# Performance work log

Measured on AMD Instinct MI355X. Metric: run time of the kernel, lower is better.

Reference implementation:

```python
import jax, jax.numpy as jnp
import numpy as np

CODEBOOK_SIZE = 1024
EMBED_DIM = 256
LEVELS = 8
N_TOKENS = 65536


def setup_inputs() -> dict:
    key = jax.random.key(0)
    kx, kc = jax.random.split(key)
    x = jax.random.normal(kx, (N_TOKENS, EMBED_DIM), dtype=jnp.float32)
    # L codebooks, each [K, D], matching nn.Embedding default N(0,1) init
    codebooks = jax.random.normal(kc, (LEVELS, CODEBOOK_SIZE, EMBED_DIM), dtype=jnp.float32)
    return {"x": x, "codebooks": codebooks}


def reference(x, codebooks):
    # x: [N, D]; codebooks: [L, K, D]
    # Residual VQ: per level, nearest codebook entry via squared L2,
    # using the GEMM expansion ||r||^2 + ||c||^2 - 2 r.c (same argmin as
    # the naive broadcasted (r - c)^2 sum, without the [N, K, D] tensor).
    levels = codebooks.shape[0]
    residual = x
    quantized = jnp.zeros_like(x)
    codes = []
    for l in range(levels):
        cb = codebooks[l]                                  # [K, D]
        r_sq = jnp.sum(residual * residual, axis=1, keepdims=True)   # [N, 1]
        c_sq = jnp.sum(cb * cb, axis=1)[None, :]                      # [1, K]
        cross = jnp.einsum('nd,kd->nk', residual, cb)                 # [N, K]
        dists = r_sq + c_sq - 2.0 * cross                              # [N, K]
        idx = jnp.argmin(dists, axis=1)                                # [N]
        codes.append(idx)
        quant = cb[idx]                                                # [N, D]
        quantized = quantized + quant
        residual = residual - quant
    return quantized, jnp.stack(codes, axis=1)  # [N, D], [N, L]
```

## Files before the change

kernel.cpp:

```cpp
#include <hip/hip_runtime.h>

#define N_TOK 65536
#define DIM   256
#define KCB   1024
#define LVL   8
#define TPB   32
#define THREADS 1024
#define CAND_MAX 32
#define MARGIN_STAR 0.6f
#define MARGIN_F32  0.125f
#define RPAD  258

typedef __attribute__((ext_vector_type(8))) short bf16x8;
typedef __attribute__((ext_vector_type(4))) float f32x4;

static __device__ inline unsigned short f2bf(float f) {
    unsigned u = __float_as_uint(f);
    unsigned r = u + 0x7FFFu + ((u >> 16) & 1u);
    return (unsigned short)(r >> 16);
}

static __device__ inline unsigned fflip(float x) {
    unsigned u = __float_as_uint(x);
    return (u & 0x80000000u) ? ~u : (u | 0x80000000u);
}
static __device__ inline float funflip(unsigned u) {
    return __uint_as_float((u & 0x80000000u) ? (u & 0x7FFFFFFFu) : ~u);
}

__device__ __noinline__ double dist64(const double* r, const float* crow) {
    double s0 = 0.0, s1 = 0.0, s2 = 0.0, s3 = 0.0;
    #pragma unroll 8
    for (int d = 0; d < DIM; d += 4) {
        float4 c = *(const float4*)(crow + d);
        double a = r[d]     - (double)c.x;
        double b = r[d + 1] - (double)c.y;
        double e = r[d + 2] - (double)c.z;
        double f = r[d + 3] - (double)c.w;
        s0 += a * a; s1 += b * b; s2 += e * e; s3 += f * f;
    }
    return (s0 + s1) + (s2 + s3);
}

__global__ void pack_kernel(const float* __restrict__ cb, short* __restrict__ packed) {
    const int lane = threadIdx.x & 63;
    const int fid  = (blockIdx.x * blockDim.x + threadIdx.x) >> 6;
    const int l  = fid >> 9;
    const int n  = (fid >> 3) & 63;
    const int kk = fid & 7;
    const int col = n * 16 + (lane & 15);
    const int kb  = kk * 32 + (lane >> 4) * 8;
    const float* src = cb + ((long)(l * KCB + col)) * DIM + kb;
    float4 f0 = *(const float4*)src;
    float4 f1 = *(const float4*)(src + 4);
    float fv[8] = {f0.x, f0.y, f0.z, f0.w, f1.x, f1.y, f1.z, f1.w};
    union { unsigned short s[8]; int4 v; } H;
    #pragma unroll
    for (int j = 0; j < 8; j++) H.s[j] = f2bf(fv[j]);
    *(int4*)(packed + (long)fid * 512 + lane * 8) = H.v;
}

__global__ void bias_kernel(const float* __restrict__ cb, float* __restrict__ bias) {
    const int lane = threadIdx.x & 63;
    const int wid  = (blockIdx.x * blockDim.x + threadIdx.x) >> 6;
    const int nw   = (gridDim.x * blockDim.x) >> 6;
    for (int row = wid; row < LVL * KCB; row += nw) {
        float4 c = *(const float4*)(cb + (long)row * DIM + lane * 4);
        float s = c.x * c.x + c.y * c.y + c.z * c.z + c.w * c.w;
        for (int off = 32; off; off >>= 1) s += __shfl_xor(s, off);
        if (lane == 0) bias[row] = -0.5f * s;
    }
}

__global__ __launch_bounds__(THREADS, 4) void rvq_mfma(const float* __restrict__ x,
                                                       const float* __restrict__ cb,
                                                       const short* __restrict__ packed,
                                                       const float* __restrict__ bias,
                                                       float* __restrict__ out) {
    __shared__ short    abufH[2 * 8 * 64 * 8];
    __shared__ float    bias_s[KCB];
    __shared__ unsigned maxu[TPB];
    __shared__ int      ccnt[TPB];
    __shared__ int      clist[TPB][CAND_MAX];
    __shared__ int      codes_s[TPB][LVL];

    const int tid  = threadIdx.x;
    const int w    = tid >> 6;
    const int lane = tid & 63;
    const int tokq = tid >> 5;
    const int c32  = tid & 31;
    const long tok0 = (long)blockIdx.x * TPB;
    const float* xblk = x + tok0 * DIM;

    double res[8];
    #pragma unroll
    for (int p = 0; p < 4; p++) {
        float2 xv = *(const float2*)(xblk + tokq * DIM + 2 * c32 + 64 * p);
        res[2 * p]     = (double)xv.x;
        res[2 * p + 1] = (double)xv.y;
    }
    if (tid < TPB) { ccnt[tid] = 0; maxu[tid] = 0u; }
    bias_s[tid] = bias[tid];

    bf16x8 chA[4], chB[4];
    {
        const short* pack0 = packed + ((long)(w * 4) * 8) * 512 + lane * 8;
        #pragma unroll
        for (int n = 0; n < 4; n++) chA[n] = *(const bf16x8*)(pack0 + (long)(n * 8 + 0) * 512);
        #pragma unroll
        for (int n = 0; n < 4; n++) chB[n] = *(const bf16x8*)(pack0 + (long)(n * 8 + 1) * 512);
    }
    {
        const int m = tokq >> 4, tr = tokq & 15;
        #pragma unroll
        for (int p = 0; p < 4; p++) {
            int d = 2 * c32 + 64 * p;
            unsigned short hA = f2bf((float)res[2 * p]);
            unsigned short hB = f2bf((float)res[2 * p + 1]);
            int kk  = d >> 5;
            int ls  = tr + ((d >> 3) & 3) * 16;
            int idx = ((m * 8 + kk) * 64 + ls) * 8 + (d & 7);
            *(unsigned*)&abufH[idx] = (unsigned)hA | ((unsigned)hB << 16);
        }
    }
    __syncthreads();

    for (int l = 0; l < LVL; l++) {
        const float* cbl = cb + (long)l * KCB * DIM;

        const short* packW = packed + ((long)(l * 64 + w * 4) * 8) * 512 + lane * 8;
        f32x4 acc[2][4];
        #pragma unroll
        for (int n = 0; n < 4; n++) {
            float b = bias_s[w * 64 + n * 16 + (lane & 15)];
            acc[0][n] = (f32x4){b, b, b, b};
            acc[1][n] = (f32x4){b, b, b, b};
        }
        #pragma unroll
        for (int kk2 = 0; kk2 < 8; kk2 += 2) {
            {
                bf16x8 ah0 = *(const bf16x8*)(abufH + (kk2)     * 512 + lane * 8);
                bf16x8 ah1 = *(const bf16x8*)(abufH + (8 + kk2) * 512 + lane * 8);
                #pragma unroll
                for (int n = 0; n < 4; n++) {
                    acc[0][n] = __builtin_amdgcn_mfma_f32_16x16x32_bf16(ah0, chA[n], acc[0][n], 0, 0, 0);
                    acc[1][n] = __builtin_amdgcn_mfma_f32_16x16x32_bf16(ah1, chA[n], acc[1][n], 0, 0, 0);
                }
            }
            if (kk2 + 2 < 8) {
                #pragma unroll
                for (int n = 0; n < 4; n++)
                    chA[n] = *(const bf16x8*)(packW + (long)(n * 8 + kk2 + 2) * 512);
            }
            {
                bf16x8 ah0 = *(const bf16x8*)(abufH + (kk2 + 1) * 512 + lane * 8);
                bf16x8 ah1 = *(const bf16x8*)(abufH + (9 + kk2) * 512 + lane * 8);
                #pragma unroll
                for (int n = 0; n < 4; n++) {
                    acc[0][n] = __builtin_amdgcn_mfma_f32_16x16x32_bf16(ah0, chB[n], acc[0][n], 0, 0, 0);
                    acc[1][n] = __builtin_amdgcn_mfma_f32_16x16x32_bf16(ah1, chB[n], acc[1][n], 0, 0, 0);
                }
            }
            if (kk2 + 3 < 8) {
                #pragma unroll
                for (int n = 0; n < 4; n++)
                    chB[n] = *(const bf16x8*)(packW + (long)(n * 8 + kk2 + 3) * 512);
            }
        }

        {
            float bv[2][4];
            #pragma unroll
            for (int m = 0; m < 2; m++)
                #pragma unroll
                for (int r = 0; r < 4; r++) {
                    float v = acc[m][0][r];
                    #pragma unroll
                    for (int n = 1; n < 4; n++) v = fmaxf(v, acc[m][n][r]);
                    bv[m][r] = v;
                }
            #pragma unroll
            for (int off = 1; off < 16; off <<= 1)
                #pragma unroll
                for (int m = 0; m < 2; m++)
                    #pragma unroll
                    for (int r = 0; r < 4; r++)
                        bv[m][r] = fmaxf(bv[m][r], __shfl_xor(bv[m][r], off));
            if ((lane & 15) == 0)
                #pragma unroll
                for (int m = 0; m < 2; m++)
                    #pragma unroll
                    for (int r = 0; r < 4; r++)
                        atomicMax(&maxu[m * 16 + (lane >> 4) * 4 + r], fflip(bv[m][r]));
        }
        __syncthreads();

        #pragma unroll
        for (int m = 0; m < 2; m++)
            #pragma unroll
            for (int r = 0; r < 4; r++) {
                int tok = m * 16 + (lane >> 4) * 4 + r;
                float thr = funflip(maxu[tok]) - MARGIN_STAR;
                #pragma unroll
                for (int n = 0; n < 4; n++) {
                    if (acc[m][n][r] >= thr) {
                        int k = w * 64 + n * 16 + (lane & 15);
                        int pos = atomicAdd(&ccnt[tok], 1);
                        if (pos < CAND_MAX) clist[tok][pos] = k;
                    }
                }
            }
        __syncthreads();

        {
            const int lp = (l + 1 < LVL) ? l + 1 : l;
            const short* packN = packed + ((long)(lp * 64 + w * 4) * 8) * 512 + lane * 8;
            #pragma unroll
            for (int n = 0; n < 4; n++) chA[n] = *(const bf16x8*)(packN + (long)(n * 8 + 0) * 512);
            #pragma unroll
            for (int n = 0; n < 4; n++) chB[n] = *(const bf16x8*)(packN + (long)(n * 8 + 1) * 512);
            if (l + 1 < LVL) bias_s[tid] = bias[(l + 1) * KCB + tid];
        }
        int cnt = ccnt[tokq];
        if (cnt > CAND_MAX) cnt = CAND_MAX;
        if (c32 == 0) { ccnt[tokq] = 0; maxu[tokq] = 0u; }
        int bk;
        if (cnt == 1) {
            bk = clist[tokq][0];
        } else {
            double bd = 1e300; bk = KCB;
            for (int j = 0; j < cnt; j++) {
                int k = clist[tokq][j];
                const float* crow = cbl + (long)k * DIM + 2 * c32;
                double s = 0.0;
                #pragma unroll
                for (int p = 0; p < 4; p++) {
                    float2 cv = *(const float2*)(crow + 64 * p);
                    double a  = res[2 * p]     - (double)cv.x;
                    double b2 = res[2 * p + 1] - (double)cv.y;
                    s += a * a + b2 * b2;
                }
                #pragma unroll
                for (int off = 1; off < 32; off <<= 1) s += __shfl_xor(s, off);
                if (s < bd || (s == bd && k < bk)) { bd = s; bk = k; }
            }
        }
        if (c32 == 0) codes_s[tokq][l] = bk;
        {
            const float* crow = cbl + (long)bk * DIM + 2 * c32;
            #pragma unroll
            for (int p = 0; p < 4; p++) {
                float2 cv = *(const float2*)(crow + 64 * p);
                res[2 * p]     -= (double)cv.x;
                res[2 * p + 1] -= (double)cv.y;
            }
        }
        {
            const int m = tokq >> 4, tr = tokq & 15;
            #pragma unroll
            for (int p = 0; p < 4; p++) {
                int d = 2 * c32 + 64 * p;
                unsigned short hA = f2bf((float)res[2 * p]);
                unsigned short hB = f2bf((float)res[2 * p + 1]);
                int kk  = d >> 5;
                int ls  = tr + ((d >> 3) & 3) * 16;
                int idx = ((m * 8 + kk) * 64 + ls) * 8 + (d & 7);
                *(unsigned*)&abufH[idx] = (unsigned)hA | ((unsigned)hB << 16);
            }
        }
        __syncthreads();
    }

    #pragma unroll
    for (int p = 0; p < 4; p++) {
        int d = 2 * c32 + 64 * p;
        float2 xv = *(const float2*)(xblk + tokq * DIM + d);
        float2 q;
        q.x = (float)((double)xv.x - res[2 * p]);
        q.y = (float)((double)xv.y - res[2 * p + 1]);
        *(float2*)(out + (tok0 + tokq) * DIM + d) = q;
    }
    float* cout = out + (long)N_TOK * DIM;
    if (tid < TPB * LVL) {
        int t = tid >> 3, ll = tid & 7;
        cout[(tok0 + t) * LVL + ll] = (float)codes_s[t][ll];
    }
}

__global__ void csq_kernel(const float* __restrict__ cb, float* __restrict__ csq) {
    const int lane = threadIdx.x & 63;
    const int wid  = (blockIdx.x * blockDim.x + threadIdx.x) >> 6;
    const int nw   = (gridDim.x * blockDim.x) >> 6;
    for (int row = wid; row < LVL * KCB; row += nw) {
        float4 c = *(const float4*)(cb + (long)row * DIM + lane * 4);
        float s = c.x * c.x + c.y * c.y + c.z * c.z + c.w * c.w;
        for (int off = 32; off; off >>= 1) s += __shfl_xor(s, off);
        if (lane == 0) csq[row] = s;
    }
}

__global__ __launch_bounds__(256) void rvq_kernel(const float* __restrict__ x,
                                                  const float* __restrict__ cb,
                                                  const float* __restrict__ csq,
                                                  float* __restrict__ out) {
    __shared__ double r64[16 * RPAD];
    __shared__ float  r32[16 * DIM];
    __shared__ float  wval[4][16];
    __shared__ float  minv[16];
    __shared__ unsigned long long dbits[16];
    __shared__ int    dmin_idx[16];
    __shared__ int    codes_s2[16][LVL];

    const int tid  = threadIdx.x;
    const int wave = tid >> 6;
    const int lane = tid & 63;
    const long tok0 = (long)blockIdx.x * 16;
    const float* xblk = x + tok0 * DIM;

    for (int i = 0; i < 16; i++) {
        float v = xblk[i * DIM + tid];
        r64[i * RPAD + tid] = (double)v;
        r32[i * DIM + tid] = v;
    }
    __syncthreads();

    const int k0 = wave * 256 + lane * 4;
    for (int l = 0; l < LVL; l++) {
        const float* cbl = cb + (long)l * KCB * DIM;
        float acc[4][16];
        #pragma unroll
        for (int j = 0; j < 4; j++)
            #pragma unroll
            for (int t = 0; t < 16; t++) acc[j][t] = 0.f;
        for (int d0 = 0; d0 < DIM; d0 += 4) {
            float4 c4[4];
            #pragma unroll
            for (int j = 0; j < 4; j++)
                c4[j] = *(const float4*)(cbl + (long)(k0 + j) * DIM + d0);
            #pragma unroll
            for (int t = 0; t < 16; t++) {
                float4 r4 = *(const float4*)(r32 + t * DIM + d0);
                #pragma unroll
                for (int j = 0; j < 4; j++) {
                    acc[j][t] = fmaf(c4[j].x, r4.x, acc[j][t]);
                    acc[j][t] = fmaf(c4[j].y, r4.y, acc[j][t]);
                    acc[j][t] = fmaf(c4[j].z, r4.z, acc[j][t]);
                    acc[j][t] = fmaf(c4[j].w, r4.w, acc[j][t]);
                }
            }
        }
        float cs[4];
        #pragma unroll
        for (int j = 0; j < 4; j++) cs[j] = csq[l * KCB + k0 + j];
        #pragma unroll
        for (int j = 0; j < 4; j++)
            #pragma unroll
            for (int t = 0; t < 16; t++)
                acc[j][t] = cs[j] - 2.0f * acc[j][t];

        #pragma unroll
        for (int t = 0; t < 16; t++) {
            float bv = acc[0][t];
            #pragma unroll
            for (int j = 1; j < 4; j++) bv = fminf(bv, acc[j][t]);
            for (int off = 1; off < 64; off <<= 1) bv = fminf(bv, __shfl_xor(bv, off));
            if (lane == 0) wval[wave][t] = bv;
        }
        __syncthreads();
        if (tid < 16) {
            float m = wval[0][tid];
            for (int ww = 1; ww < 4; ww++) m = fminf(m, wval[ww][tid]);
            minv[tid] = m;
            dbits[tid] = 0xFFFFFFFFFFFFFFFFULL;
            dmin_idx[tid] = KCB;
        }
        __syncthreads();
        #pragma unroll
        for (int t = 0; t < 16; t++) {
            float thr = minv[t] + MARGIN_F32;
            #pragma unroll
            for (int j = 0; j < 4; j++)
                if (acc[j][t] <= thr) {
                    double d64 = dist64(r64 + t * RPAD, cbl + (long)(k0 + j) * DIM);
                    atomicMin(&dbits[t], (unsigned long long)__double_as_longlong(d64));
                }
        }
        __syncthreads();
        #pragma unroll
        for (int t = 0; t < 16; t++) {
            float thr = minv[t] + MARGIN_F32;
            #pragma unroll
            for (int j = 0; j < 4; j++)
                if (acc[j][t] <= thr) {
                    double d64 = dist64(r64 + t * RPAD, cbl + (long)(k0 + j) * DIM);
                    if ((unsigned long long)__double_as_longlong(d64) == dbits[t])
                        atomicMin(&dmin_idx[t], k0 + j);
                }
        }
        __syncthreads();
        if (tid < 16) codes_s2[tid][l] = dmin_idx[tid];
        for (int i = 0; i < 16; i++) {
            int k = dmin_idx[i];
            float c = cbl[(long)k * DIM + tid];
            double nr = r64[i * RPAD + tid] - (double)c;
            r64[i * RPAD + tid] = nr;
            r32[i * DIM + tid] = (float)nr;
        }
        __syncthreads();
    }
    for (int i = 0; i < 16; i++) {
        double q = (double)xblk[i * DIM + tid] - r64[i * RPAD + tid];
        out[tok0 * DIM + i * DIM + tid] = (float)q;
    }
    float* cout = out + (long)N_TOK * DIM;
    if (tid < 16 * LVL) {
        int t = tid >> 3, ll = tid & 7;
        cout[(tok0 + t) * LVL + ll] = (float)codes_s2[t][ll];
    }
}

extern "C" void kernel_launch(void* const* d_in, const int* in_sizes, int n_in,
                              void* d_out, int out_size, void* d_ws, size_t ws_size,
                              hipStream_t stream) {
    const float* x  = (const float*)d_in[0];
    const float* cb = (const float*)d_in[1];
    const size_t need = (size_t)4 * 1024 * 1024 + 32 * 1024;
    if (ws_size >= need) {
        short* packed = (short*)d_ws;
        float* bias = (float*)((char*)d_ws + (size_t)4 * 1024 * 1024);
        pack_kernel<<<1024, 256, 0, stream>>>(cb, packed);
        bias_kernel<<<32, 256, 0, stream>>>(cb, bias);
        rvq_mfma<<<N_TOK / TPB, THREADS, 0, stream>>>(x, cb, packed, bias, (float*)d_out);
    } else {
        float* csq = (float*)d_ws;
        csq_kernel<<<32, 256, 0, stream>>>(cb, csq);
        rvq_kernel<<<N_TOK / 16, 256, 0, stream>>>(x, cb, csq, (float*)d_out);
    }
}
```

Measured before the change: 748.4 us.

## Replace block-wide max atomics with per-wave candidate lists and score-based filtering

Drops the block-wide atomicMax pass and one __syncthreads per level. Each wave now thresholds candidates against its own local max and stores (score, index) pairs in per-wave lists capped at six entries. The refine stage takes the global max from the stored scores, re-filters, and checks only the survivors in fp64. If any wave list overflows, it falls back to a brute-force scan of all 1024 codes. Codebook fragments are no longer prefetched for the next level, which may expose global load latency, and the cap-overflow fallback could be very costly if it triggers often.

```diff
diff --git a/kernel.cpp b/kernel.cpp
--- a/kernel.cpp
+++ b/kernel.cpp
@@ -6,7 +6,7 @@
 #define LVL   8
 #define TPB   32
 #define THREADS 1024
-#define CAND_MAX 32
+#define CAP   6
 #define MARGIN_STAR 0.6f
 #define MARGIN_F32  0.125f
 #define RPAD  258
@@ -18,14 +18,6 @@
     unsigned u = __float_as_uint(f);
     unsigned r = u + 0x7FFFu + ((u >> 16) & 1u);
     return (unsigned short)(r >> 16);
-}
-
-static __device__ inline unsigned fflip(float x) {
-    unsigned u = __float_as_uint(x);
-    return (u & 0x80000000u) ? ~u : (u | 0x80000000u);
-}
-static __device__ inline float funflip(unsigned u) {
-    return __uint_as_float((u & 0x80000000u) ? (u & 0x7FFFFFFFu) : ~u);
 }
 
 __device__ __noinline__ double dist64(const double* r, const float* crow) {
@@ -77,12 +69,11 @@
                                                        const short* __restrict__ packed,
                                                        const float* __restrict__ bias,
                                                        float* __restrict__ out) {
-    __shared__ short    abufH[2 * 8 * 64 * 8];
-    __shared__ float    bias_s[KCB];
-    __shared__ unsigned maxu[TPB];
-    __shared__ int      ccnt[TPB];
-    __shared__ int      clist[TPB][CAND_MAX];
-    __shared__ int      codes_s[TPB][LVL];
+    __shared__ short              abufH[2 * 8 * 64 * 8];
+    __shared__ float              bias_s[KCB];
+    __shared__ int                cntw[16][TPB];
+    __shared__ unsigned long long listw[16][TPB][CAP];
+    __shared__ int                codes_s[TPB][LVL];
 
     const int tid  = threadIdx.x;
     const int w    = tid >> 6;
@@ -99,17 +90,9 @@
         res[2 * p]     = (double)xv.x;
         res[2 * p + 1] = (double)xv.y;
     }
-    if (tid < TPB) { ccnt[tid] = 0; maxu[tid] = 0u; }
+    if (tid < 512) cntw[tid >> 5][tid & 31] = 0;
     bias_s[tid] = bias[tid];
 
-    bf16x8 chA[4], chB[4];
-    {
-        const short* pack0 = packed + ((long)(w * 4) * 8) * 512 + lane * 8;
-        #pragma unroll
-        for (int n = 0; n < 4; n++) chA[n] = *(const bf16x8*)(pack0 + (long)(n * 8 + 0) * 512);
-        #pragma unroll
-        for (int n = 0; n < 4; n++) chB[n] = *(const bf16x8*)(pack0 + (long)(n * 8 + 1) * 512);
-    }
     {
         const int m = tokq >> 4, tr = tokq & 15;
         #pragma unroll
@@ -129,6 +112,11 @@
         const float* cbl = cb + (long)l * KCB * DIM;
 
         const short* packW = packed + ((long)(l * 64 + w * 4) * 8) * 512 + lane * 8;
+        bf16x8 chA[4], chB[4];
+        #pragma unroll
+        for (int n = 0; n < 4; n++) chA[n] = *(const bf16x8*)(packW + (long)(n * 8 + 0) * 512);
+        #pragma unroll
+        for (int n = 0; n < 4; n++) chB[n] = *(const bf16x8*)(packW + (long)(n * 8 + 1) * 512);
         f32x4 acc[2][4];
         #pragma unroll
         for (int n = 0; n < 4; n++) {
@@ -186,51 +174,46 @@
                     #pragma unroll
                     for (int r = 0; r < 4; r++)
                         bv[m][r] = fmaxf(bv[m][r], __shfl_xor(bv[m][r], off));
-            if ((lane & 15) == 0)
-                #pragma unroll
-                for (int m = 0; m < 2; m++)
+            #pragma unroll
+            for (int m = 0; m < 2; m++)
+                #pragma unroll
+                for (int r = 0; r < 4; r++) {
+                    int tok = m * 16 + (lane >> 4) * 4 + r;
+                    float thr = bv[m][r] - MARGIN_STAR;
                     #pragma unroll
-                    for (int r = 0; r < 4; r++)
-                        atomicMax(&maxu[m * 16 + (lane >> 4) * 4 + r], fflip(bv[m][r]));
-        }
-        __syncthreads();
-
-        #pragma unroll
-        for (int m = 0; m < 2; m++)
-            #pragma unroll
-            for (int r = 0; r < 4; r++) {
-                int tok = m * 16 + (lane >> 4) * 4 + r;
-                float thr = funflip(maxu[tok]) - MARGIN_STAR;
-                #pragma unroll
-                for (int n = 0; n < 4; n++) {
-                    if (acc[m][n][r] >= thr) {
-                        int k = w * 64 + n * 16 + (lane & 15);
-                        int pos = atomicAdd(&ccnt[tok], 1);
-                        if (pos < CAND_MAX) clist[tok][pos] = k;
+                    for (int n = 0; n < 4; n++) {
+                        if (acc[m][n][r] >= thr) {
+                            int k = w * 64 + n * 16 + (lane & 15);
+                            int pos = atomicAdd(&cntw[w][tok], 1);
+                            if (pos < CAP)
+                                listw[w][tok][pos] =
+                                    ((unsigned long long)__float_as_uint(acc[m][n][r]) << 32) | (unsigned)k;
+                        }
                     }
                 }
-            }
-        __syncthreads();
-
-        {
-            const int lp = (l + 1 < LVL) ? l + 1 : l;
-            const short* packN = packed + ((long)(lp * 64 + w * 4) * 8) * 512 + lane * 8;
-            #pragma unroll
-            for (int n = 0; n < 4; n++) chA[n] = *(const bf16x8*)(packN + (long)(n * 8 + 0) * 512);
-            #pragma unroll
-            for (int n = 0; n < 4; n++) chB[n] = *(const bf16x8*)(packN + (long)(n * 8 + 1) * 512);
-            if (l + 1 < LVL) bias_s[tid] = bias[(l + 1) * KCB + tid];
-        }
-        int cnt = ccnt[tokq];
-        if (cnt > CAND_MAX) cnt = CAND_MAX;
-        if (c32 == 0) { ccnt[tokq] = 0; maxu[tokq] = 0u; }
+        }
+        __syncthreads();
+
+        int rawc = (c32 < 16) ? cntw[c32][tokq] : 0;
+        int cc   = rawc > CAP ? CAP : rawc;
+        if (c32 < 16) cntw[c32][tokq] = 0;
+        unsigned long long cnts = 0;
+        #pragma unroll
+        for (int i = 0; i < 16; i++) {
+            int ci = __shfl(cc, i, 32);
+            cnts |= (unsigned long long)(ci & 7) << (3 * i);
+        }
+        int ov = (rawc > CAP) ? 1 : 0;
+        #pragma unroll
+        for (int off = 1; off < 32; off <<= 1) ov |= __shfl_xor(ov, off);
+        int total = 0;
+        #pragma unroll
+        for (int i = 0; i < 16; i++) total += (int)((cnts >> (3 * i)) & 7);
+
         int bk;
-        if (cnt == 1) {
-            bk = clist[tokq][0];
-        } else {
+        if (ov) {
             double bd = 1e300; bk = KCB;
-            for (int j = 0; j < cnt; j++) {
-                int k = clist[tokq][j];
+            for (int k = 0; k < KCB; k++) {
                 const float* crow = cbl + (long)k * DIM + 2 * c32;
                 double s = 0.0;
                 #pragma unroll
@@ -242,30 +225,64 @@
                 }
                 #pragma unroll
                 for (int off = 1; off < 32; off <<= 1) s += __shfl_xor(s, off);
-                if (s < bd || (s == bd && k < bk)) { bd = s; bk = k; }
+                if (s < bd) { bd = s; bk = k; }
+            }
+        } else if (total == 1) {
+            bk = KCB;
+            for (int wv = 0; wv < 16; wv++)
+                if ((cnts >> (3 * wv)) & 7) { bk = (int)(listw[wv][tokq][0] & 0xFFFFFFFFu); break; }
+        } else {
+            float lmax = -1e30f;
+            if (c32 < 16)
+                for (int j = 0; j < cc; j++)
+                    lmax = fmaxf(lmax, __uint_as_float((unsigned)(listw[c32][tokq][j] >> 32)));
+            #pragma unroll
+            for (int off = 1; off < 32; off <<= 1) lmax = fmaxf(lmax, __shfl_xor(lmax, off));
+            float thr = lmax - MARGIN_STAR;
+            double bd = 1e300; bk = KCB;
+            for (int wv = 0; wv < 16; wv++) {
+                int cw = (int)((cnts >> (3 * wv)) & 7);
+                for (int j = 0; j < cw; j++) {
+                    unsigned long long e = listw[wv][tokq][j];
+                    float sc = __uint_as_float((unsigned)(e >> 32));
+                    if (sc >= thr) {
+                        int k = (int)(e & 0xFFFFFFFFu);
+                        const float* crow = cbl + (long)k * DIM + 2 * c32;
+                        double s = 0.0;
+                        #pragma unroll
+                        for (int p = 0; p < 4; p++) {
+                            float2 cv = *(const float2*)(crow + 64 * p);
+                            double a  = res[2 * p]     - (double)cv.x;
+                            double b2 = res[2 * p + 1] - (double)cv.y;
+                            s += a * a + b2 * b2;
+                        }
+                        #pragma unroll
+                        for (int off = 1; off < 32; off <<= 1) s += __shfl_xor(s, off);
+                        if (s < bd || (s == bd && k < bk)) { bd = s; bk = k; }
+                    }
+                }
             }
         }
         if (c32 == 0) codes_s[tokq][l] = bk;
+
+        if (l + 1 < LVL) bias_s[tid] = bias[(l + 1) * KCB + tid];
         {
             const float* crow = cbl + (long)bk * DIM + 2 * c32;
+            const int m = tokq >> 4, tr = tokq & 15;
             #pragma unroll
             for (int p = 0; p < 4; p++) {
                 float2 cv = *(const float2*)(crow + 64 * p);
                 res[2 * p]     -= (double)cv.x;
                 res[2 * p + 1] -= (double)cv.y;
-            }
-        }
-        {
-            const int m = tokq >> 4, tr = tokq & 15;
-            #pragma unroll
-            for (int p = 0; p < 4; p++) {
-                int d = 2 * c32 + 64 * p;
-                unsigned short hA = f2bf((float)res[2 * p]);
-                unsigned short hB = f2bf((float)res[2 * p + 1]);
-                int kk  = d >> 5;
-                int ls  = tr + ((d >> 3) & 3) * 16;
-                int idx = ((m * 8 + kk) * 64 + ls) * 8 + (d & 7);
-                *(unsigned*)&abufH[idx] = (unsigned)hA | ((unsigned)hB << 16);
+                if (l + 1 < LVL) {
+                    int d = 2 * c32 + 64 * p;
+                    unsigned short hA = f2bf((float)res[2 * p]);
+                    unsigned short hB = f2bf((float)res[2 * p + 1]);
+                    int kk  = d >> 5;
+                    int ls  = tr + ((d >> 3) & 3) * 16;
+                    int idx = ((m * 8 + kk) * 64 + ls) * 8 + (d & 7);
+                    *(unsigned*)&abufH[idx] = (unsigned)hA | ((unsigned)hB << 16);
+                }
             }
         }
         __syncthreads();
```

Result: slower. 1.105 ms (+47.6%).
